# Kernel optimization log

Hardware: AMD Instinct MI355X
Metric: run time of the kernel (lower is better)

The kernel has to match this reference:

```python
import jax, jax.numpy as jnp
import numpy as np

LMAX = 6
F_IN, F_OUT = 64, 64
N_ROT = 64  # n_angles**3
IRREP_FLAT = sum((2 * l + 1) ** 2 for l in range(LMAX + 1))  # 455
BATCH = 1024


def setup_inputs() -> dict:
    key = jax.random.key(0)
    k_x, k_d, k_w = jax.random.split(key, 3)
    x = jax.random.normal(k_x, (BATCH, F_IN, IRREP_FLAT), dtype=jnp.float32)
    D = jax.random.normal(k_d, (N_ROT, IRREP_FLAT), dtype=jnp.float32)  # flat Wigner-D buffer
    w = jax.random.normal(k_w, (F_IN, F_OUT, N_ROT), dtype=jnp.float32)
    return {"x": x, "D": D, "w": w}


def reference(x, D, w):
    B, f_in, _ = x.shape
    f_out = w.shape[1]
    n_rot = D.shape[0]
    # psi[f,g,i] = sum_n D[n,i] * w[f,g,n] / sqrt(N)
    psi = jnp.einsum('ni,fgn->fgi', D, w) / jnp.sqrt(jnp.asarray(n_rot, x.dtype))
    outs = []
    off = 0
    for l in range(LMAX + 1):
        d = 2 * l + 1          # irrep dim == multiplicity for so3_irreps
        blk = d * d
        # weight block: (f_in, f_out, mul_in=u, mul_out=v)
        Wl = psi[:, :, off:off + blk].reshape(f_in, f_out, d, d)
        # input block: (B, f_in, mul=u, irrep_dim=m)
        xl = x[:, :, off:off + blk].reshape(B, f_in, d, d)
        # e3nn Linear path norm ('element'): 1/sqrt(f_in * mul_in)
        norm = 1.0 / np.sqrt(f_in * d)
        yl = jnp.einsum('bfum,fguv->bgvm', xl, Wl) * norm
        outs.append(yl.reshape(B, f_out, blk))
        off += blk
    return jnp.concatenate(outs, axis=-1)  # (B, f_out, 455)
```

## Files before the change

### kernel.cpp

```cpp
#include <hip/hip_runtime.h>
#include <stdint.h>


typedef __bf16 bf16x8 __attribute__((ext_vector_type(8)));
typedef float floatx4 __attribute__((ext_vector_type(4)));

#define XROW 29120

__device__ __forceinline__ unsigned short f2bf(float f) {
  union { float f; unsigned int u; } c; c.f = f;
  unsigned int u = c.u;
  return (unsigned short)((u + 0x7FFFu + ((u >> 16) & 1u)) >> 16);
}
__device__ __forceinline__ unsigned int pack2(float a, float b) {
  return (unsigned int)f2bf(a) | ((unsigned int)f2bf(b) << 16);
}

__host__ __device__ constexpr int d_of(int L) { return 2 * L + 1; }
__host__ __device__ constexpr int off_of(int L) { int s = 0; for (int i = 0; i < L; ++i) s += d_of(i) * d_of(i); return s; }
__host__ __device__ constexpr size_t a_off(int L) { size_t s = 0; for (int i = 0; i < L; ++i) s += (size_t)65536 * d_of(i) * d_of(i); return s; }
__host__ __device__ constexpr size_t b_off(int L) { size_t s = a_off(7); for (int i = 0; i < L; ++i) s += (size_t)4096 * d_of(i) * (d_of(i) + 1); return s; }

__global__ __launch_bounds__(256) void prep(const float* __restrict__ x, const float* __restrict__ Dm,
                                            const float* __restrict__ w, unsigned short* __restrict__ ws) {
  __shared__ __align__(16) float smem[64 * 68 + 64 * 172];
  const int tid = threadIdx.x;
  const int bid = blockIdx.x;

  if (bid < 448) {
    float* wg = smem;
    float* Dl = smem + 64 * 68;
    const int g = bid & 63, l = bid >> 6;
    const int d = 2 * l + 1, d2 = d * d, K = 64 * d;
    int off = 0; size_t boff = a_off(7);
    for (int i = 0; i < l; ++i) { int dd = 2 * i + 1; off += dd * dd; boff += (size_t)4096 * dd * (dd + 1); }
    unsigned short* B = ws + boff;

    for (int t = tid; t < 4096; t += 256) {
      int n = t & 63, f = t >> 6;
      wg[n * 68 + f] = w[(size_t)f * 4096 + g * 64 + n];
    }
    for (int t = tid; t < 64 * 172; t += 256) {
      int n = t / 172, r = t - n * 172;
      Dl[t] = (r < d2) ? Dm[n * 455 + off + r] : 0.f;
    }
    __syncthreads();

    const float sl = 1.0f / (64.0f * sqrtf((float)d));
    const int RT = (d2 + 3) >> 2;
    for (int tt = tid; tt < 16 * RT; tt += 256) {
      const int ft = tt & 15, rt = tt >> 4;
      float acc[4][4] = {};
      for (int n = 0; n < 64; ++n) {
        floatx4 wv = *(const floatx4*)(wg + n * 68 + ft * 4);
        floatx4 dv = *(const floatx4*)(Dl + n * 172 + rt * 4);
#pragma unroll
        for (int a = 0; a < 4; ++a)
#pragma unroll
          for (int b2 = 0; b2 < 4; ++b2) acc[a][b2] += wv[a] * dv[b2];
      }
#pragma unroll
      for (int b2 = 0; b2 < 4; ++b2) {
        int r = rt * 4 + b2;
        if (r < d2) {
          int u = r / d, v = r - u * d;
          size_t base = (size_t)(g * d + v) * K + u * 64 + ft * 4;
#pragma unroll
          for (int a = 0; a < 4; ++a) B[base + a] = f2bf(acc[a][b2] * sl);
        }
      }
    }
    {
      int nn = 64 * d + g;
      for (int k = tid; k < K; k += 256) B[(size_t)nn * K + k] = 0;
    }
  } else {
    float* xs = smem;
    const int b = bid - 448;
    const float* xb = x + (size_t)b * XROW;
    size_t aoff = 0;

    for (int t = tid; t < 64 * 165; t += 256) { int f = t / 165, c = t - f * 165; xs[t] = xb[(size_t)f * 455 + c]; }
    __syncthreads();
    int off = 0;
#pragma unroll
    for (int l = 0; l < 5; ++l) {
      const int d = 2 * l + 1, d2 = d * d, n1 = 64 * d2;
      unsigned int* A = (unsigned int*)(ws + aoff + (size_t)b * n1);
      for (int t = tid; t < (n1 >> 1); t += 256) {
        int f2 = t & 31, s = t >> 5;
        int u = s % d, m = s / d;
        int c = off + u * d + m;
        A[t] = pack2(xs[(2 * f2) * 165 + c], xs[(2 * f2 + 1) * 165 + c]);
      }
      off += d2; aoff += (size_t)1024 * n1;
    }
    __syncthreads();
    for (int t = tid; t < 64 * 121; t += 256) { int f = t / 121, c = t - f * 121; xs[t] = xb[(size_t)f * 455 + 165 + c]; }
    __syncthreads();
    {
      const int n1 = 64 * 121;
      unsigned int* A = (unsigned int*)(ws + aoff + (size_t)b * n1);
      for (int t = tid; t < (n1 >> 1); t += 256) {
        int f2 = t & 31, s = t >> 5;
        int u = s % 11, m = s / 11;
        int c = u * 11 + m;
        A[t] = pack2(xs[(2 * f2) * 121 + c], xs[(2 * f2 + 1) * 121 + c]);
      }
      aoff += (size_t)1024 * n1;
    }
    __syncthreads();
    for (int t = tid; t < 64 * 169; t += 256) { int f = t / 169, c = t - f * 169; xs[t] = xb[(size_t)f * 455 + 286 + c]; }
    __syncthreads();
    {
      const int n1 = 64 * 169;
      unsigned int* A = (unsigned int*)(ws + aoff + (size_t)b * n1);
      for (int t = tid; t < (n1 >> 1); t += 256) {
        int f2 = t & 31, s = t >> 5;
        int u = s % 13, m = s / 13;
        int c = u * 13 + m;
        A[t] = pack2(xs[(2 * f2) * 169 + c], xs[(2 * f2 + 1) * 169 + c]);
      }
    }
  }
}

__device__ __forceinline__ void async_copy16(const void* gp, void* lp) {
  __builtin_amdgcn_global_load_lds((__attribute__((address_space(1))) void*)gp,
                                   (__attribute__((address_space(3))) void*)lp, 16, 0, 0);
}

template <int L>
__device__ __forceinline__ void gemm_body(int local, const unsigned short* __restrict__ ws,
                                          float* __restrict__ out,
                                          unsigned short* As, unsigned short* Bs) {
  constexpr int d = 2 * L + 1;
  constexpr int K = 64 * d;
  constexpr int NT = (d + 1) / 2;
  constexpr int OFF = off_of(L);
  const unsigned short* A = ws + a_off(L);
  const unsigned short* B = ws + b_off(L);
  const int x8 = local & 7, tt = local >> 3;
  const int mt = (tt / NT) * 8 + x8;
  const int nt = tt % NT;
  const int tid = threadIdx.x;
  const int w = tid >> 6, ln = tid & 63;
  const int wm = w >> 1, wn = w & 1;
  const int q = ln >> 4, r16 = ln & 15;

  const unsigned short* gp[4];
  unsigned short* ldst[4];
#pragma unroll
  for (int i = 0; i < 4; ++i) {
    int c = i * 256 + tid;
    if (i < 2) {
      gp[i] = A + (size_t)(mt * 128 + (c >> 2)) * K + (c & 3) * 8;
      ldst[i] = As + (i * 256 + w * 64) * 8;
    } else {
      int c2 = c - 512;
      gp[i] = B + (size_t)(nt * 128 + (c2 >> 2)) * K + (c2 & 3) * 8;
      ldst[i] = Bs + ((i - 2) * 256 + w * 64) * 8;
    }
  }

  const int aoffs0 = (wm * 64 + r16) * 32 + q * 8;
  const int boffs0 = (wn * 64 + r16) * 32 + q * 8;

  floatx4 acc[4][4] = {};

  for (int kt = 0; kt < 2 * d; ++kt) {
    __syncthreads();
#pragma unroll
    for (int i = 0; i < 4; ++i) async_copy16(gp[i], ldst[i]);
    __syncthreads();
    bf16x8 af[4], bfr[4];
#pragma unroll
    for (int mi = 0; mi < 4; ++mi) af[mi] = *(const bf16x8*)(As + aoffs0 + mi * 512);
#pragma unroll
    for (int ni = 0; ni < 4; ++ni) bfr[ni] = *(const bf16x8*)(Bs + boffs0 + ni * 512);
#pragma unroll
    for (int mi = 0; mi < 4; ++mi)
#pragma unroll
      for (int ni = 0; ni < 4; ++ni)
        acc[mi][ni] = __builtin_amdgcn_mfma_f32_16x16x32_bf16(af[mi], bfr[ni], acc[mi][ni], 0, 0, 0);
#pragma unroll
    for (int i = 0; i < 4; ++i) gp[i] += 32;
  }

#pragma unroll
  for (int ni = 0; ni < 4; ++ni) {
    int Cc = nt * 128 + wn * 64 + ni * 16 + r16;
    if (Cc < 64 * d) {
      int g = Cc / d, v = Cc - (Cc / d) * d;
#pragma unroll
      for (int mi = 0; mi < 4; ++mi) {
        int R0 = mt * 128 + wm * 64 + mi * 16 + q * 4;
#pragma unroll
        for (int reg = 0; reg < 4; ++reg) {
          int R = R0 + reg;
          int bb = R / d, m = R - (R / d) * d;
          out[(size_t)bb * XROW + g * 455 + OFF + v * d + m] = acc[mi][ni][reg];
        }
      }
    }
  }
}

__global__ __launch_bounds__(256) void gemm_all(const unsigned short* __restrict__ ws, float* __restrict__ out) {
  __shared__ alignas(16) unsigned short As[128 * 32];
  __shared__ alignas(16) unsigned short Bs[128 * 32];
  int b0 = 2015 - (int)blockIdx.x;
  if      (b0 <    8) gemm_body<0>(b0,        ws, out, As, Bs);
  else if (b0 <   56) gemm_body<1>(b0 -    8, ws, out, As, Bs);
  else if (b0 <  176) gemm_body<2>(b0 -   56, ws, out, As, Bs);
  else if (b0 <  400) gemm_body<3>(b0 -  176, ws, out, As, Bs);
  else if (b0 <  760) gemm_body<4>(b0 -  400, ws, out, As, Bs);
  else if (b0 < 1288) gemm_body<5>(b0 -  760, ws, out, As, Bs);
  else                gemm_body<6>(b0 - 1288, ws, out, As, Bs);
}

extern "C" void kernel_launch(void* const* d_in, const int* in_sizes, int n_in,
                              void* d_out, int out_size, void* d_ws, size_t ws_size,
                              hipStream_t stream) {
  const float* x = (const float*)d_in[0];
  const float* D = (const float*)d_in[1];
  const float* w = (const float*)d_in[2];
  float* out = (float*)d_out;
  unsigned short* ws = (unsigned short*)d_ws;

  hipLaunchKernelGGL(prep, dim3(1472), dim3(256), 0, stream, x, D, w, ws);
  hipLaunchKernelGGL(gemm_all, dim3(2016), dim3(256), 0, stream, ws, out);
}
```

Baseline: 367.2 us.

## Load GEMM fragments directly from global with register double-buffering; vectorize x repack

```diff
diff --git a/kernel.cpp b/kernel.cpp
--- a/kernel.cpp
+++ b/kernel.cpp
@@ -78,66 +78,37 @@
     float* xs = smem;
     const int b = bid - 448;
     const float* xb = x + (size_t)b * XROW;
-    size_t aoff = 0;
-
-    for (int t = tid; t < 64 * 165; t += 256) { int f = t / 165, c = t - f * 165; xs[t] = xb[(size_t)f * 455 + c]; }
-    __syncthreads();
-    int off = 0;
 #pragma unroll
-    for (int l = 0; l < 5; ++l) {
-      const int d = 2 * l + 1, d2 = d * d, n1 = 64 * d2;
-      unsigned int* A = (unsigned int*)(ws + aoff + (size_t)b * n1);
-      for (int t = tid; t < (n1 >> 1); t += 256) {
-        int f2 = t & 31, s = t >> 5;
-        int u = s % d, m = s / d;
-        int c = off + u * d + m;
-        A[t] = pack2(xs[(2 * f2) * 165 + c], xs[(2 * f2 + 1) * 165 + c]);
+    for (int h = 0; h < 2; ++h) {
+      const float4* src = (const float4*)(xb + h * 32 * 455);
+      for (int t = tid; t < 3640; t += 256) ((float4*)xs)[t] = src[t];
+      __syncthreads();
+      size_t aoff = 0; int off = 0;
+#pragma unroll
+      for (int l = 0; l < 7; ++l) {
+        const int d = 2 * l + 1, d2 = d * d;
+        unsigned int* Au = (unsigned int*)(ws + aoff + (size_t)b * (64 * d2));
+        for (int t = tid; t < 16 * d2; t += 256) {
+          int f2 = t & 15, s = t >> 4;
+          int u = s % d, m = s / d;
+          int c = off + u * d + m;
+          Au[s * 32 + h * 16 + f2] = pack2(xs[(2 * f2) * 455 + c], xs[(2 * f2 + 1) * 455 + c]);
+        }
+        off += d2; aoff += (size_t)1024 * 64 * d2;
       }
-      off += d2; aoff += (size_t)1024 * n1;
-    }
-    __syncthreads();
-    for (int t = tid; t < 64 * 121; t += 256) { int f = t / 121, c = t - f * 121; xs[t] = xb[(size_t)f * 455 + 165 + c]; }
-    __syncthreads();
-    {
-      const int n1 = 64 * 121;
-      unsigned int* A = (unsigned int*)(ws + aoff + (size_t)b * n1);
-      for (int t = tid; t < (n1 >> 1); t += 256) {
-        int f2 = t & 31, s = t >> 5;
-        int u = s % 11, m = s / 11;
-        int c = u * 11 + m;
-        A[t] = pack2(xs[(2 * f2) * 121 + c], xs[(2 * f2 + 1) * 121 + c]);
-      }
-      aoff += (size_t)1024 * n1;
-    }
-    __syncthreads();
-    for (int t = tid; t < 64 * 169; t += 256) { int f = t / 169, c = t - f * 169; xs[t] = xb[(size_t)f * 455 + 286 + c]; }
-    __syncthreads();
-    {
-      const int n1 = 64 * 169;
-      unsigned int* A = (unsigned int*)(ws + aoff + (size_t)b * n1);
-      for (int t = tid; t < (n1 >> 1); t += 256) {
-        int f2 = t & 31, s = t >> 5;
-        int u = s % 13, m = s / 13;
-        int c = u * 13 + m;
-        A[t] = pack2(xs[(2 * f2) * 169 + c], xs[(2 * f2 + 1) * 169 + c]);
-      }
+      __syncthreads();
     }
   }
 }
 
-__device__ __forceinline__ void async_copy16(const void* gp, void* lp) {
-  __builtin_amdgcn_global_load_lds((__attribute__((address_space(1))) void*)gp,
-                                   (__attribute__((address_space(3))) void*)lp, 16, 0, 0);
-}
-
 template <int L>
 __device__ __forceinline__ void gemm_body(int local, const unsigned short* __restrict__ ws,
-                                          float* __restrict__ out,
-                                          unsigned short* As, unsigned short* Bs) {
+                                          float* __restrict__ out) {
   constexpr int d = 2 * L + 1;
   constexpr int K = 64 * d;
   constexpr int NT = (d + 1) / 2;
   constexpr int OFF = off_of(L);
+  constexpr int ITERS = 2 * d;
   const unsigned short* A = ws + a_off(L);
   const unsigned short* B = ws + b_off(L);
   const int x8 = local & 7, tt = local >> 3;
@@ -148,44 +119,38 @@
   const int wm = w >> 1, wn = w & 1;
   const int q = ln >> 4, r16 = ln & 15;
 
-  const unsigned short* gp[4];
-  unsigned short* ldst[4];
+  const unsigned short* ap = A + (size_t)(mt * 128 + wm * 64 + r16) * K + q * 8;
+  const unsigned short* bp = B + (size_t)(nt * 128 + wn * 64 + r16) * K + q * 8;
+
+  floatx4 acc[4][4] = {};
+  bf16x8 ca[4], cb[4], na[4], nb[4];
 #pragma unroll
   for (int i = 0; i < 4; ++i) {
-    int c = i * 256 + tid;
-    if (i < 2) {
-      gp[i] = A + (size_t)(mt * 128 + (c >> 2)) * K + (c & 3) * 8;
-      ldst[i] = As + (i * 256 + w * 64) * 8;
-    } else {
-      int c2 = c - 512;
-      gp[i] = B + (size_t)(nt * 128 + (c2 >> 2)) * K + (c2 & 3) * 8;
-      ldst[i] = Bs + ((i - 2) * 256 + w * 64) * 8;
+    ca[i] = *(const bf16x8*)(ap + i * 16 * K);
+    cb[i] = *(const bf16x8*)(bp + i * 16 * K);
+  }
+#pragma unroll 2
+  for (int kt = 0; kt < ITERS - 1; ++kt) {
+    const unsigned short* ap2 = ap + (kt + 1) * 32;
+    const unsigned short* bp2 = bp + (kt + 1) * 32;
+#pragma unroll
+    for (int i = 0; i < 4; ++i) {
+      na[i] = *(const bf16x8*)(ap2 + i * 16 * K);
+      nb[i] = *(const bf16x8*)(bp2 + i * 16 * K);
     }
-  }
-
-  const int aoffs0 = (wm * 64 + r16) * 32 + q * 8;
-  const int boffs0 = (wn * 64 + r16) * 32 + q * 8;
-
-  floatx4 acc[4][4] = {};
-
-  for (int kt = 0; kt < 2 * d; ++kt) {
-    __syncthreads();
-#pragma unroll
-    for (int i = 0; i < 4; ++i) async_copy16(gp[i], ldst[i]);
-    __syncthreads();
-    bf16x8 af[4], bfr[4];
-#pragma unroll
-    for (int mi = 0; mi < 4; ++mi) af[mi] = *(const bf16x8*)(As + aoffs0 + mi * 512);
-#pragma unroll
-    for (int ni = 0; ni < 4; ++ni) bfr[ni] = *(const bf16x8*)(Bs + boffs0 + ni * 512);
 #pragma unroll
     for (int mi = 0; mi < 4; ++mi)
 #pragma unroll
       for (int ni = 0; ni < 4; ++ni)
-        acc[mi][ni] = __builtin_amdgcn_mfma_f32_16x16x32_bf16(af[mi], bfr[ni], acc[mi][ni], 0, 0, 0);
+        acc[mi][ni] = __builtin_amdgcn_mfma_f32_16x16x32_bf16(ca[mi], cb[ni], acc[mi][ni], 0, 0, 0);
 #pragma unroll
-    for (int i = 0; i < 4; ++i) gp[i] += 32;
+    for (int i = 0; i < 4; ++i) { ca[i] = na[i]; cb[i] = nb[i]; }
   }
+#pragma unroll
+  for (int mi = 0; mi < 4; ++mi)
+#pragma unroll
+    for (int ni = 0; ni < 4; ++ni)
+      acc[mi][ni] = __builtin_amdgcn_mfma_f32_16x16x32_bf16(ca[mi], cb[ni], acc[mi][ni], 0, 0, 0);
 
 #pragma unroll
   for (int ni = 0; ni < 4; ++ni) {
@@ -207,16 +172,14 @@
 }
 
 __global__ __launch_bounds__(256) void gemm_all(const unsigned short* __restrict__ ws, float* __restrict__ out) {
-  __shared__ alignas(16) unsigned short As[128 * 32];
-  __shared__ alignas(16) unsigned short Bs[128 * 32];
   int b0 = 2015 - (int)blockIdx.x;
-  if      (b0 <    8) gemm_body<0>(b0,        ws, out, As, Bs);
-  else if (b0 <   56) gemm_body<1>(b0 -    8, ws, out, As, Bs);
-  else if (b0 <  176) gemm_body<2>(b0 -   56, ws, out, As, Bs);
-  else if (b0 <  400) gemm_body<3>(b0 -  176, ws, out, As, Bs);
-  else if (b0 <  760) gemm_body<4>(b0 -  400, ws, out, As, Bs);
-  else if (b0 < 1288) gemm_body<5>(b0 -  760, ws, out, As, Bs);
-  else                gemm_body<6>(b0 - 1288, ws, out, As, Bs);
+  if      (b0 <    8) gemm_body<0>(b0,        ws, out);
+  else if (b0 <   56) gemm_body<1>(b0 -    8, ws, out);
+  else if (b0 <  176) gemm_body<2>(b0 -   56, ws, out);
+  else if (b0 <  400) gemm_body<3>(b0 -  176, ws, out);
+  else if (b0 <  760) gemm_body<4>(b0 -  400, ws, out);
+  else if (b0 < 1288) gemm_body<5>(b0 -  760, ws, out);
+  else                gemm_body<6>(b0 - 1288, ws, out);
 }
 
 extern "C" void kernel_launch(void* const* d_in, const int* in_sizes, int n_in,
```

After: 454.6 us. 23.8% more time.
